# Performance work log

Measured on AMD Instinct MI355X. Metric: run time of the kernel, lower is better.

## Reference

```python
import math
import jax, jax.numpy as jnp
import numpy as np

B, N, C = 2, 2048, 1024
H = 16
D = C // H  # 64
LN_EPS = 1e-5


def setup_inputs() -> dict:
    key = jax.random.key(0)
    ks = jax.random.split(key, 5)
    x = jax.random.normal(ks[0], (B, N, C), dtype=jnp.float32)
    w_qkv = jax.random.normal(ks[1], (C, 3 * C), dtype=jnp.float32) * 0.02
    w_proj = jax.random.normal(ks[2], (C, C), dtype=jnp.float32) * 0.02
    b_proj = jnp.zeros((C,), dtype=jnp.float32)
    ln_w = jnp.ones((D,), dtype=jnp.float32) + jax.random.normal(ks[3], (D,), dtype=jnp.float32) * 0.02
    ln_b = jax.random.normal(ks[4], (D,), dtype=jnp.float32) * 0.02
    return {"x": x, "w_qkv": w_qkv, "w_proj": w_proj, "b_proj": b_proj,
            "ln_w": ln_w, "ln_b": ln_b}


def _layernorm(t, w, b):
    mu = jnp.mean(t, axis=-1, keepdims=True)
    var = jnp.var(t, axis=-1, keepdims=True)
    return (t - mu) * jax.lax.rsqrt(var + LN_EPS) * w + b


def reference(x, w_qkv, w_proj, b_proj, ln_w, ln_b):
    b, n, c = x.shape
    h, d = H, c // H
    # QKV projection (no bias): [b,n,3c] -> [3,b,h,n,d]
    qkv = (x @ w_qkv).reshape(b, n, 3, h, d).transpose(2, 0, 3, 1, 4)
    q, k, v = qkv[0], qkv[1], qkv[2]
    # per-head LayerNorm on q and k (qk_norm)
    q = _layernorm(q, ln_w, ln_b)
    k = _layernorm(k, ln_w, ln_b)
    # NOTE: source multiplies q by sqrt(head_dim) (faithful to original)
    q = q * jnp.asarray(math.sqrt(d), dtype=q.dtype)
    scores = jnp.einsum('bhnd,bhmd->bhnm', q, k)  # [b,h,n,n]
    mask_value = -jnp.finfo(scores.dtype).max
    causal = jnp.tril(jnp.ones((n, n), dtype=bool))
    scores = jnp.where(causal, scores, mask_value)
    attn = jax.nn.softmax(scores, axis=-1)
    out = jnp.einsum('bhnm,bhmd->bhnd', attn, v)  # [b,h,n,d]
    out = out.transpose(0, 2, 1, 3).reshape(b, n, c)  # b n (h d)
    return out @ w_proj + b_proj
```

## Files before the change

### kernel.cpp

```cpp
#include <hip/hip_runtime.h>

#define LOG2E 1.4426950408889634f

typedef _Float16 f16x8_t __attribute__((ext_vector_type(8)));
typedef _Float16 f16x4_t __attribute__((ext_vector_type(4)));
typedef _Float16 f16x2_t __attribute__((ext_vector_type(2)));
typedef float    f32x4_t __attribute__((ext_vector_type(4)));

#define MFMA32(a, b, c) __builtin_amdgcn_mfma_f32_16x16x32_f16(a, b, c, 0, 0, 0)
#define MFMA16(a, b, c) __builtin_amdgcn_mfma_f32_16x16x16f16(a, b, c, 0, 0, 0)

__device__ __forceinline__ void async_copy16(void* lds, const void* g) {
    __builtin_amdgcn_global_load_lds(
        (const __attribute__((address_space(1))) unsigned char*)g,
        (__attribute__((address_space(3))) unsigned char*)lds, 16, 0, 0);
}

__global__ void prep_k(const float* __restrict__ x, _Float16* __restrict__ xh,
                       const float* __restrict__ wq, _Float16* __restrict__ wqT,
                       const float* __restrict__ wp, _Float16* __restrict__ wpT) {
    __shared__ _Float16 tl[64][65];
    const int bx = blockIdx.x, t = threadIdx.x;
    if (bx < 4096) {
        const int i = bx * 256 + t;
        float4 v = ((const float4*)x)[i];
        f16x4_t o = { (_Float16)v.x, (_Float16)v.y, (_Float16)v.z, (_Float16)v.w };
        ((f16x4_t*)xh)[i] = o;
        return;
    }
    const float* in; _Float16* out; int C, bxx, byy;
    if (bx < 4864) { const int id = bx - 4096; in = wq; out = wqT; C = 3072; bxx = id % 48; byy = id / 48; }
    else           { const int id = bx - 4864; in = wp; out = wpT; C = 1024; bxx = id % 16; byy = id / 16; }
    const int R = 1024;
    const int c = t & 63;
    const int r4 = t >> 6;
    const int r0 = byy * 64, c0 = bxx * 64;
#pragma unroll
    for (int i = 0; i < 16; ++i) {
        int r = r4 + i * 4;
        tl[c][r] = (_Float16)in[(size_t)(r0 + r) * C + c0 + c];
    }
    __syncthreads();
#pragma unroll
    for (int i = 0; i < 16; ++i) {
        int rr = r4 + i * 4;
        out[(size_t)(c0 + rr) * R + r0 + c] = tl[rr][c];
    }
}

__global__ void vtrans_k(const _Float16* __restrict__ qkv, _Float16* __restrict__ VTg) {
    __shared__ _Float16 tl[64][68];
    const int tid = threadIdx.x;
    const int bh = blockIdx.x;
    const int b = bh >> 4, h = bh & 15;
    const int t = blockIdx.y;
    const int c = tid & 63;
    const int r4 = tid >> 6;
#pragma unroll
    for (int i = 0; i < 16; ++i) {
        int r = r4 + i * 4;
        tl[c][r] = qkv[(size_t)(b * 2048 + t * 64 + r) * 3072 + 2048 + h * 64 + c];
    }
    __syncthreads();
    const size_t obase = (size_t)bh * 131072 + (size_t)t * 4096;
#pragma unroll
    for (int e = 0; e < 2; ++e) {
        const int ci = tid * 2 + e;
        const int d = ci >> 3, w = ci & 7;
        const int pq = w ^ (d & 7);
        const int base = (pq >> 2) * 32 + (pq & 3) * 4;
        f16x4_t v0 = *(const f16x4_t*)&tl[d][base];
        f16x4_t v1 = *(const f16x4_t*)&tl[d][base + 16];
        f16x8_t val = __builtin_shufflevector(v0, v1, 0, 1, 2, 3, 4, 5, 6, 7);
        *(f16x8_t*)&VTg[obase + ci * 8] = val;
    }
}

template <typename OutT, bool BIAS, bool LNQK>
__global__ __launch_bounds__(256, 3)
void gemm_f16_k(const _Float16* __restrict__ A, const _Float16* __restrict__ BT,
                OutT* __restrict__ C, const float* __restrict__ bias,
                const float* __restrict__ ln_w, const float* __restrict__ ln_b,
                int M, int N, int K) {
    __shared__ _Float16 As[2][128][32];
    __shared__ _Float16 Bs[2][128][32];
    const int tid = threadIdx.x;
    const int wid = tid >> 6, lane = tid & 63;
    const int qd = lane >> 4, ln = lane & 15;
    const int m0 = blockIdx.x * 128, n0 = blockIdx.y * 128;
    const int wm = (wid >> 1) * 64, wn = (wid & 1) * 64;

    f32x4_t acc[4][4] = {};

    const int srow = lane >> 2;
    const int skk  = (lane & 3) * 8;

    for (int k0 = 0; k0 < K; k0 += 64) {
        __syncthreads();
#pragma unroll
        for (int p = 0; p < 4; ++p) {
            const int seg = p * 4 + wid;
            const int s   = seg >> 3;
            const int rg  = seg & 7;
            const int row = rg * 16 + srow;
            const size_t goff = (size_t)row * K + k0 + s * 32 + skk;
            async_copy16(&As[0][0][0] + seg * 512, A  + (size_t)m0 * K + goff);
            async_copy16(&Bs[0][0][0] + seg * 512, BT + (size_t)n0 * K + goff);
        }
        __syncthreads();
#pragma unroll
        for (int s = 0; s < 2; ++s) {
            f16x8_t a[4], b[4];
#pragma unroll
            for (int i = 0; i < 4; ++i)
                a[i] = *(const f16x8_t*)&As[s][wm + i * 16 + ln][qd * 8];
#pragma unroll
            for (int j = 0; j < 4; ++j)
                b[j] = *(const f16x8_t*)&Bs[s][wn + j * 16 + ln][qd * 8];
#pragma unroll
            for (int i = 0; i < 4; ++i)
#pragma unroll
                for (int j = 0; j < 4; ++j)
                    acc[i][j] = MFMA32(a[i], b[j], acc[i][j]);
        }
    }

    if constexpr (LNQK) {
        if (n0 < 2048) {
            const float scale = (n0 < 1024) ? 8.0f * LOG2E : 1.0f;
            float lw[4], lb[4];
#pragma unroll
            for (int j = 0; j < 4; ++j) { lw[j] = ln_w[j * 16 + ln]; lb[j] = ln_b[j * 16 + ln]; }
#pragma unroll
            for (int i = 0; i < 4; ++i)
#pragma unroll
                for (int r = 0; r < 4; ++r) {
                    float s = acc[i][0][r] + acc[i][1][r] + acc[i][2][r] + acc[i][3][r];
                    s += __shfl_xor(s, 1); s += __shfl_xor(s, 2);
                    s += __shfl_xor(s, 4); s += __shfl_xor(s, 8);
                    const float mu = s * 0.015625f;
                    const float d0 = acc[i][0][r] - mu, d1 = acc[i][1][r] - mu;
                    const float d2 = acc[i][2][r] - mu, d3 = acc[i][3][r] - mu;
                    float v = d0 * d0 + d1 * d1 + d2 * d2 + d3 * d3;
                    v += __shfl_xor(v, 1); v += __shfl_xor(v, 2);
                    v += __shfl_xor(v, 4); v += __shfl_xor(v, 8);
                    const float rs = rsqrtf(v * 0.015625f + 1e-5f);
                    acc[i][0][r] = (d0 * rs * lw[0] + lb[0]) * scale;
                    acc[i][1][r] = (d1 * rs * lw[1] + lb[1]) * scale;
                    acc[i][2][r] = (d2 * rs * lw[2] + lb[2]) * scale;
                    acc[i][3][r] = (d3 * rs * lw[3] + lb[3]) * scale;
                }
        }
    }

#pragma unroll
    for (int i = 0; i < 4; ++i)
#pragma unroll
        for (int j = 0; j < 4; ++j) {
            const int col = n0 + wn + j * 16 + ln;
            const float bv = BIAS ? bias[col] : 0.0f;
#pragma unroll
            for (int r = 0; r < 4; ++r) {
                const int row = m0 + wm + i * 16 + qd * 4 + r;
                C[(size_t)row * N + col] = (OutT)(acc[i][j][r] + bv);
            }
        }
}

__global__ __launch_bounds__(256, 2)
void gemm_f16_m64_k(const _Float16* __restrict__ A, const _Float16* __restrict__ BT,
                    float* __restrict__ C, const float* __restrict__ bias,
                    int M, int N, int K) {
    __shared__ _Float16 As[2][64][32];
    __shared__ _Float16 Bs[2][128][32];
    const int tid = threadIdx.x;
    const int wid = tid >> 6, lane = tid & 63;
    const int qd = lane >> 4, ln = lane & 15;
    const int m0 = blockIdx.x * 64, n0 = blockIdx.y * 128;
    const int wn = wid * 32;

    f32x4_t acc[4][2] = {};
    const int srow = lane >> 2;
    const int skk  = (lane & 3) * 8;

    for (int k0 = 0; k0 < K; k0 += 64) {
        __syncthreads();
#pragma unroll
        for (int p = 0; p < 2; ++p) {
            const int seg = p * 4 + wid;
            const int hidx = seg * 512 + lane * 8;
            const int s_ = hidx >> 11;
            const int row = (hidx >> 5) & 63;
            const int kk = hidx & 31;
            async_copy16(&As[0][0][0] + seg * 512,
                         A + (size_t)(m0 + row) * K + k0 + s_ * 32 + kk);
        }
#pragma unroll
        for (int p = 0; p < 4; ++p) {
            const int seg = p * 4 + wid;
            const int s   = seg >> 3;
            const int rg  = seg & 7;
            const int row = rg * 16 + srow;
            async_copy16(&Bs[0][0][0] + seg * 512,
                         BT + (size_t)(n0 + row) * K + k0 + s * 32 + skk);
        }
        __syncthreads();
#pragma unroll
        for (int s = 0; s < 2; ++s) {
            f16x8_t a[4], b[2];
#pragma unroll
            for (int i = 0; i < 4; ++i)
                a[i] = *(const f16x8_t*)&As[s][i * 16 + ln][qd * 8];
#pragma unroll
            for (int j = 0; j < 2; ++j)
                b[j] = *(const f16x8_t*)&Bs[s][wn + j * 16 + ln][qd * 8];
#pragma unroll
            for (int i = 0; i < 4; ++i)
#pragma unroll
                for (int j = 0; j < 2; ++j)
                    acc[i][j] = MFMA32(a[i], b[j], acc[i][j]);
        }
    }
#pragma unroll
    for (int i = 0; i < 4; ++i)
#pragma unroll
        for (int j = 0; j < 2; ++j) {
            const int col = n0 + wn + j * 16 + ln;
            const float bv = bias[col];
#pragma unroll
            for (int r = 0; r < 4; ++r) {
                const int row = m0 + i * 16 + qd * 4 + r;
                C[(size_t)row * N + col] = acc[i][j][r] + bv;
            }
        }
}

__global__ __launch_bounds__(256, 3)
void attn_part_k(const _Float16* __restrict__ qkv, const _Float16* __restrict__ VTg,
                 _Float16* __restrict__ O, float* __restrict__ Op, float* __restrict__ ml) {
    __shared__ _Float16 Ks[2][2][64][32];
    __shared__ _Float16 VT[2][64][64];

    const int tid = threadIdx.x;
    const int wid = tid >> 6, lane = tid & 63;
    const int qd = lane >> 4, ln = lane & 15;
    const int bh = blockIdx.x;
    const int b = bh >> 4, h = bh & 15;
    const int y = blockIdx.y;
    int band, chunk, nst;
    if (y < 8)       { band = 8 + y;  chunk = 0; nst = 16; }
    else if (y < 16) { band = 23 - y; chunk = 1; nst = 2 * band - 14; }
    else             { band = y - 16; chunk = 0; nst = 2 * band + 2; }
    const size_t vtbase = (size_t)bh * 131072;
    const int qrow0 = band * 128 + wid * 32;
    const int kvbeg = chunk * 1024;

    f16x8_t qf[2][2];
#pragma unroll
    for (int qt = 0; qt < 2; ++qt)
#pragma unroll
        for (int s = 0; s < 2; ++s)
            qf[qt][s] = *(const f16x8_t*)&qkv[(size_t)(b * 2048 + qrow0 + qt * 16 + ln) * 3072
                                             + h * 64 + s * 32 + qd * 8];

    f32x4_t o[2][4] = {};
    f32x4_t ls[2] = {};
    float m[2] = { -3.0e38f, -3.0e38f };
    const f16x4_t ones = { (_Float16)1.0f, (_Float16)1.0f, (_Float16)1.0f, (_Float16)1.0f };

    auto stage = [&](int buf, int kv0) {
#pragma unroll
        for (int p = 0; p < 2; ++p) {
            const int seg = p * 4 + wid;
            const int hidx = seg * 512 + lane * 8;
            const int s_ = hidx >> 11;
            const int rrow = (hidx >> 5) & 63;
            const int kk = hidx & 31;
            async_copy16(&Ks[buf][0][0][0] + seg * 512,
                         qkv + (size_t)(b * 2048 + kv0 + rrow) * 3072 + 1024 + h * 64
                             + s_ * 32 + kk);
        }
#pragma unroll
        for (int p = 0; p < 2; ++p) {
            const int seg = p * 4 + wid;
            async_copy16(&VT[buf][0][0] + seg * 512,
                         VTg + vtbase + (size_t)kv0 * 64 + seg * 512 + lane * 8);
        }
    };

    stage(0, kvbeg);

    for (int st = 0; st < nst; ++st) {
        const int kv0 = kvbeg + st * 64;
        __syncthreads();
        if (st + 1 < nst) stage((st + 1) & 1, kv0 + 64);
        const int buf = st & 1;

        if (kv0 <= qrow0 + 31) {
            f32x4_t sc[2][4];
#pragma unroll
            for (int jt = 0; jt < 4; ++jt) {
                f16x8_t k0 = *(const f16x8_t*)&Ks[buf][0][jt * 16 + ln][qd * 8];
                f16x8_t k1 = *(const f16x8_t*)&Ks[buf][1][jt * 16 + ln][qd * 8];
#pragma unroll
                for (int qt = 0; qt < 2; ++qt) {
                    f32x4_t s = {};
                    s = MFMA32(k0, qf[qt][0], s);
                    s = MFMA32(k1, qf[qt][1], s);
                    sc[qt][jt] = s;
                }
            }
            f16x8_t vf8[4][2];
#pragma unroll
            for (int dt = 0; dt < 4; ++dt)
#pragma unroll
                for (int pp = 0; pp < 2; ++pp) {
                    const int w = (pp * 4 + qd) ^ (ln & 7);
                    vf8[dt][pp] = *(const f16x8_t*)&VT[buf][dt * 16 + ln][w * 8];
                }

#pragma unroll
            for (int qt = 0; qt < 2; ++qt) {
                if (kv0 + 63 > qrow0 + qt * 16) {
                    const int qq = qrow0 + qt * 16 + ln;
#pragma unroll
                    for (int c = 0; c < 4; ++c)
#pragma unroll
                        for (int r = 0; r < 4; ++r)
                            if (kv0 + c * 16 + qd * 4 + r > qq) sc[qt][c][r] = -3.0e38f;
                }
                f32x4_t mq = sc[qt][0];
#pragma unroll
                for (int c = 1; c < 4; ++c)
#pragma unroll
                    for (int r = 0; r < 4; ++r) mq[r] = fmaxf(mq[r], sc[qt][c][r]);
                float mx = fmaxf(fmaxf(mq[0], mq[1]), fmaxf(mq[2], mq[3]));
                mx = fmaxf(mx, __shfl_xor(mx, 16));
                mx = fmaxf(mx, __shfl_xor(mx, 32));
                if (!__all(mx <= m[qt] + 8.0f)) {
                    const float mn = fmaxf(m[qt], mx);
                    const float al = exp2f(m[qt] - mn);
#pragma unroll
                    for (int dt = 0; dt < 4; ++dt) o[qt][dt] *= al;
                    ls[qt][0] *= al;
                    m[qt] = mn;
                }
                f16x4_t pf[4];
#pragma unroll
                for (int c = 0; c < 4; ++c) {
                    float p0 = exp2f(sc[qt][c][0] - m[qt]);
                    float p1 = exp2f(sc[qt][c][1] - m[qt]);
                    float p2 = exp2f(sc[qt][c][2] - m[qt]);
                    float p3 = exp2f(sc[qt][c][3] - m[qt]);
                    f16x2_t a = __builtin_bit_cast(f16x2_t, __builtin_amdgcn_cvt_pkrtz(p0, p1));
                    f16x2_t bb = __builtin_bit_cast(f16x2_t, __builtin_amdgcn_cvt_pkrtz(p2, p3));
                    pf[c] = __builtin_shufflevector(a, bb, 0, 1, 2, 3);
                }
                __builtin_amdgcn_s_setprio(1);
#pragma unroll
                for (int c = 0; c < 4; ++c) ls[qt] = MFMA16(ones, pf[c], ls[qt]);
#pragma unroll
                for (int dt = 0; dt < 4; ++dt)
#pragma unroll
                    for (int pp = 0; pp < 2; ++pp) {
                        f16x4_t lo = __builtin_shufflevector(vf8[dt][pp], vf8[dt][pp], 0, 1, 2, 3);
                        f16x4_t hi = __builtin_shufflevector(vf8[dt][pp], vf8[dt][pp], 4, 5, 6, 7);
                        o[qt][dt] = MFMA16(lo, pf[pp * 2 + 0], o[qt][dt]);
                        o[qt][dt] = MFMA16(hi, pf[pp * 2 + 1], o[qt][dt]);
                    }
                __builtin_amdgcn_s_setprio(0);
            }
        }
    }

    if (band < 8) {
        const size_t base0 = ((size_t)(b * 2048 + qrow0 + ln)) * 1024 + h * 64 + qd * 4;
#pragma unroll
        for (int qt = 0; qt < 2; ++qt) {
            const float inv = 1.0f / ls[qt][0];
            const size_t base = base0 + (size_t)qt * 16 * 1024;
#pragma unroll
            for (int dt = 0; dt < 4; ++dt) {
                f16x4_t ov;
#pragma unroll
                for (int r = 0; r < 4; ++r) ov[r] = (_Float16)(o[qt][dt][r] * inv);
                *(f16x4_t*)&O[base + dt * 16] = ov;
            }
        }
    } else {
        const size_t pb = ((size_t)bh * 8 + (band - 8)) * 2 + chunk;
#pragma unroll
        for (int qt = 0; qt < 2; ++qt) {
            const int row = wid * 32 + qt * 16 + ln;
            float* op = Op + pb * 8192 + (size_t)row * 64 + qd * 4;
#pragma unroll
            for (int dt = 0; dt < 4; ++dt)
                *(f32x4_t*)&op[dt * 16] = o[qt][dt];
            if (qd == 0) {
                ml[pb * 256 + row * 2]     = m[qt];
                ml[pb * 256 + row * 2 + 1] = ls[qt][0];
            }
        }
    }
}

__global__ __launch_bounds__(256)
void attn_merge_k(const float* __restrict__ Op, const float* __restrict__ ml,
                  _Float16* __restrict__ O) {
    const int bh = blockIdx.x, bnd = blockIdx.y;
    const int b = bh >> 4, h = bh & 15;
    const int band = 8 + bnd;
    const size_t pb = ((size_t)bh * 8 + bnd) * 2;
    const int tid = threadIdx.x;
    const int row = tid >> 1;
    const int c32 = (tid & 1) * 32;
    const float m0 = ml[pb * 256 + row * 2],       l0 = ml[pb * 256 + row * 2 + 1];
    const float m1 = ml[(pb + 1) * 256 + row * 2], l1 = ml[(pb + 1) * 256 + row * 2 + 1];
    const float mm = fmaxf(m0, m1);
    const float a0 = exp2f(m0 - mm), a1 = exp2f(m1 - mm);
    const float inv = 1.0f / (l0 * a0 + l1 * a1);
    const float* p0 = Op + pb * 8192 + (size_t)row * 64 + c32;
    const float* p1 = p0 + 8192;
    _Float16* op = O + ((size_t)(b * 2048 + band * 128 + row)) * 1024 + h * 64 + c32;
#pragma unroll
    for (int g = 0; g < 8; ++g) {
        f32x4_t v0 = *(const f32x4_t*)&p0[g * 4];
        f32x4_t v1 = *(const f32x4_t*)&p1[g * 4];
        f16x4_t ov;
#pragma unroll
        for (int r = 0; r < 4; ++r)
            ov[r] = (_Float16)((v0[r] * a0 + v1[r] * a1) * inv);
        *(f16x4_t*)&op[g * 4] = ov;
    }
}

extern "C" void kernel_launch(void* const* d_in, const int* in_sizes, int n_in,
                              void* d_out, int out_size, void* d_ws, size_t ws_size,
                              hipStream_t stream) {
    const float* x      = (const float*)d_in[0];
    const float* w_qkv  = (const float*)d_in[1];
    const float* w_proj = (const float*)d_in[2];
    const float* b_proj = (const float*)d_in[3];
    const float* ln_w   = (const float*)d_in[4];
    const float* ln_b   = (const float*)d_in[5];
    float* out = (float*)d_out;

    char* w = (char*)d_ws;
    const size_t MB = 1024 * 1024;
    _Float16*  qkv    = (_Float16*)(w);
    _Float16*  xh     = (_Float16*)(w + 24 * MB);
    _Float16*  wqkvT  = (_Float16*)(w + 32 * MB);
    _Float16*  wprojT = (_Float16*)(w + 38 * MB);
    _Float16*  VTg    = (_Float16*)(w + 40 * MB);
    _Float16*  Ah     = (_Float16*)(w + 48 * MB);
    float*     Op     = (float*)(w + 56 * MB);
    float*     mlb    = (float*)(w + 72 * MB);

    prep_k<<<5120, 256, 0, stream>>>(x, xh, w_qkv, wqkvT, w_proj, wprojT);
    gemm_f16_k<_Float16, false, true><<<dim3(32, 24), 256, 0, stream>>>(
        xh, wqkvT, qkv, nullptr, ln_w, ln_b, 4096, 3072, 1024);
    vtrans_k<<<dim3(32, 32), 256, 0, stream>>>(qkv, VTg);
    attn_part_k<<<dim3(32, 24), 256, 0, stream>>>(qkv, VTg, Ah, Op, mlb);
    attn_merge_k<<<dim3(32, 8), 256, 0, stream>>>(Op, mlb, Ah);
    gemm_f16_m64_k<<<dim3(64, 8), 256, 0, stream>>>(Ah, wprojT, out, b_proj, 4096, 1024, 1024);
}
```

Before: 194.0 us.

## Fuse V transpose into QKV GEMM epilogue and triple-buffer attention K/V loads

The separate V-transpose kernel is removed. The QKV GEMM now writes swizzled V^T directly from its accumulators through a per-wave LDS tile for column blocks at or beyond 2048, which avoids a kernel launch and a full re-read of V from global memory. The attention kernel moves from double to triple buffering of K/V tiles, using explicit vmcnt waits and raw barriers to keep two stages in flight. The row-max reduction is also reordered. This raises LDS use in attention, which could lower occupancy, and depends on the vmcnt counts being correct.

```diff
diff --git a/kernel.cpp b/kernel.cpp
--- a/kernel.cpp
+++ b/kernel.cpp
@@ -48,38 +48,11 @@
     }
 }
 
-__global__ void vtrans_k(const _Float16* __restrict__ qkv, _Float16* __restrict__ VTg) {
-    __shared__ _Float16 tl[64][68];
-    const int tid = threadIdx.x;
-    const int bh = blockIdx.x;
-    const int b = bh >> 4, h = bh & 15;
-    const int t = blockIdx.y;
-    const int c = tid & 63;
-    const int r4 = tid >> 6;
-#pragma unroll
-    for (int i = 0; i < 16; ++i) {
-        int r = r4 + i * 4;
-        tl[c][r] = qkv[(size_t)(b * 2048 + t * 64 + r) * 3072 + 2048 + h * 64 + c];
-    }
-    __syncthreads();
-    const size_t obase = (size_t)bh * 131072 + (size_t)t * 4096;
-#pragma unroll
-    for (int e = 0; e < 2; ++e) {
-        const int ci = tid * 2 + e;
-        const int d = ci >> 3, w = ci & 7;
-        const int pq = w ^ (d & 7);
-        const int base = (pq >> 2) * 32 + (pq & 3) * 4;
-        f16x4_t v0 = *(const f16x4_t*)&tl[d][base];
-        f16x4_t v1 = *(const f16x4_t*)&tl[d][base + 16];
-        f16x8_t val = __builtin_shufflevector(v0, v1, 0, 1, 2, 3, 4, 5, 6, 7);
-        *(f16x8_t*)&VTg[obase + ci * 8] = val;
-    }
-}
-
 template <typename OutT, bool BIAS, bool LNQK>
 __global__ __launch_bounds__(256, 3)
 void gemm_f16_k(const _Float16* __restrict__ A, const _Float16* __restrict__ BT,
                 OutT* __restrict__ C, const float* __restrict__ bias,
+                _Float16* __restrict__ VTg,
                 const float* __restrict__ ln_w, const float* __restrict__ ln_b,
                 int M, int N, int K) {
     __shared__ _Float16 As[2][128][32];
@@ -126,7 +99,38 @@
     }
 
     if constexpr (LNQK) {
-        if (n0 < 2048) {
+        if (n0 >= 2048) {
+            __syncthreads();
+            const int h2  = ((n0 - 2048) >> 6) + (wn >> 6);
+            const int row0 = m0 + wm;
+            const int bb  = row0 >> 11;
+            const int tt  = (row0 & 2047) >> 6;
+            const size_t obase = ((size_t)(bb * 16 + h2)) * 131072 + (size_t)tt * 4096;
+            _Float16* tlw = &As[0][0][0] + wid * 1088;
+#pragma unroll
+            for (int j = 0; j < 4; ++j) {
+#pragma unroll
+                for (int i = 0; i < 4; ++i) {
+                    f16x4_t v;
+#pragma unroll
+                    for (int r = 0; r < 4; ++r) v[r] = (_Float16)acc[i][j][r];
+                    *(f16x4_t*)&tlw[ln * 68 + i * 16 + qd * 4] = v;
+                }
+#pragma unroll
+                for (int e = 0; e < 2; ++e) {
+                    const int ci = lane * 2 + e;
+                    const int dl = ci >> 3, w2 = ci & 7;
+                    const int pq = w2 ^ (dl & 7);
+                    const int base = (pq >> 2) * 32 + (pq & 3) * 4;
+                    f16x4_t v0 = *(const f16x4_t*)&tlw[dl * 68 + base];
+                    f16x4_t v1 = *(const f16x4_t*)&tlw[dl * 68 + base + 16];
+                    f16x8_t val = __builtin_shufflevector(v0, v1, 0, 1, 2, 3, 4, 5, 6, 7);
+                    *(f16x8_t*)&VTg[obase + (size_t)((j * 16 + dl) * 8 + w2) * 8] = val;
+                }
+            }
+            return;
+        }
+        {
             const float scale = (n0 < 1024) ? 8.0f * LOG2E : 1.0f;
             float lw[4], lb[4];
 #pragma unroll
@@ -238,8 +242,8 @@
 __global__ __launch_bounds__(256, 3)
 void attn_part_k(const _Float16* __restrict__ qkv, const _Float16* __restrict__ VTg,
                  _Float16* __restrict__ O, float* __restrict__ Op, float* __restrict__ ml) {
-    __shared__ _Float16 Ks[2][2][64][32];
-    __shared__ _Float16 VT[2][64][64];
+    __shared__ _Float16 Ks[3][2][64][32];
+    __shared__ _Float16 VT[3][64][64];
 
     const int tid = threadIdx.x;
     const int wid = tid >> 6, lane = tid & 63;
@@ -289,12 +293,16 @@
     };
 
     stage(0, kvbeg);
+    stage(1, kvbeg + 64);
 
     for (int st = 0; st < nst; ++st) {
         const int kv0 = kvbeg + st * 64;
-        __syncthreads();
-        if (st + 1 < nst) stage((st + 1) & 1, kv0 + 64);
-        const int buf = st & 1;
+        if (st + 1 < nst) asm volatile("s_waitcnt vmcnt(4)" ::: "memory");
+        else              asm volatile("s_waitcnt vmcnt(0)" ::: "memory");
+        __builtin_amdgcn_s_barrier();
+        asm volatile("" ::: "memory");
+        if (st + 2 < nst) stage((st + 2) % 3, kv0 + 128);
+        const int buf = st % 3;
 
         if (kv0 <= qrow0 + 31) {
             f32x4_t sc[2][4];
@@ -329,12 +337,11 @@
                         for (int r = 0; r < 4; ++r)
                             if (kv0 + c * 16 + qd * 4 + r > qq) sc[qt][c][r] = -3.0e38f;
                 }
-                f32x4_t mq = sc[qt][0];
-#pragma unroll
-                for (int c = 1; c < 4; ++c)
-#pragma unroll
-                    for (int r = 0; r < 4; ++r) mq[r] = fmaxf(mq[r], sc[qt][c][r]);
-                float mx = fmaxf(fmaxf(mq[0], mq[1]), fmaxf(mq[2], mq[3]));
+                float mx0 = fmaxf(fmaxf(fmaxf(sc[qt][0][0], sc[qt][1][0]), sc[qt][2][0]), sc[qt][3][0]);
+                float mx1 = fmaxf(fmaxf(fmaxf(sc[qt][0][1], sc[qt][1][1]), sc[qt][2][1]), sc[qt][3][1]);
+                float mx2 = fmaxf(fmaxf(fmaxf(sc[qt][0][2], sc[qt][1][2]), sc[qt][2][2]), sc[qt][3][2]);
+                float mx3 = fmaxf(fmaxf(fmaxf(sc[qt][0][3], sc[qt][1][3]), sc[qt][2][3]), sc[qt][3][3]);
+                float mx = fmaxf(fmaxf(fmaxf(mx0, mx1), mx2), mx3);
                 mx = fmaxf(mx, __shfl_xor(mx, 16));
                 mx = fmaxf(mx, __shfl_xor(mx, 32));
                 if (!__all(mx <= m[qt] + 8.0f)) {
@@ -458,8 +465,7 @@
 
     prep_k<<<5120, 256, 0, stream>>>(x, xh, w_qkv, wqkvT, w_proj, wprojT);
     gemm_f16_k<_Float16, false, true><<<dim3(32, 24), 256, 0, stream>>>(
-        xh, wqkvT, qkv, nullptr, ln_w, ln_b, 4096, 3072, 1024);
-    vtrans_k<<<dim3(32, 32), 256, 0, stream>>>(qkv, VTg);
+        xh, wqkvT, qkv, nullptr, VTg, ln_w, ln_b, 4096, 3072, 1024);
     attn_part_k<<<dim3(32, 24), 256, 0, stream>>>(qkv, VTg, Ah, Op, mlb);
     attn_merge_k<<<dim3(32, 8), 256, 0, stream>>>(Op, mlb, Ah);
     gemm_f16_m64_k<<<dim3(64, 8), 256, 0, stream>>>(Ah, wprojT, out, b_proj, 4096, 1024, 1024);
```

Result: no change. 190.6 us (-1.8%).
